# Kernel optimization log

Hardware: AMD Instinct MI355X
Metric: run time of the kernel (lower is better)

## Reference

```python
import jax, jax.numpy as jnp
import numpy as np

Z_DIM = 64
HIDDEN = 400
DATASET = 1000000
EPS = 0.01
S_STEPS = 20
T_STEPS = 5
LOG_2PI = float(np.log(2.0 * np.pi))


def setup_inputs() -> dict:
    key = jax.random.key(0)
    ks = jax.random.split(key, 10)
    B = 16384
    x = jax.random.uniform(ks[0], (B, 1, 28, 28), dtype=jnp.float32)
    indices = jax.random.randint(ks[1], (B,), 0, DATASET, dtype=jnp.int64)
    # MLP params (torch Linear convention: y = x @ W.T + b)
    W1 = jax.random.normal(ks[2], (HIDDEN, 784), dtype=jnp.float32) * 0.03
    b1 = jnp.zeros((HIDDEN,), dtype=jnp.float32)
    W21 = jax.random.normal(ks[3], (Z_DIM, HIDDEN), dtype=jnp.float32) * 0.05
    b21 = jnp.zeros((Z_DIM,), dtype=jnp.float32)
    W22 = jax.random.normal(ks[4], (Z_DIM, HIDDEN), dtype=jnp.float32) * 0.05
    b22 = jnp.zeros((Z_DIM,), dtype=jnp.float32)
    cached_samples = jax.random.normal(ks[5], (DATASET, Z_DIM), dtype=jnp.float32)
    # pre-drawn Langevin noise for all s+t steps
    noise = jax.random.normal(ks[6], (S_STEPS + T_STEPS, B, Z_DIM), dtype=jnp.float32)
    return {"x": x, "indices": indices, "K": 1, "W1": W1, "b1": b1,
            "W21": W21, "b21": b21, "W22": W22, "b22": b22,
            "cached_samples": cached_samples, "noise": noise}


def _encode(x, W1, b1, W21, b21, W22, b22):
    xf = x.reshape(-1, 784)
    h = jax.nn.relu(xf @ W1.T + b1)
    z_loc = h @ W21.T + b21
    z_scale = jnp.exp(h @ W22.T + b22)
    return z_loc, z_scale


def _langevin(z0, noise_steps, z_loc, z_scale):
    # ULA: z <- z + eps * grad_log_q(z) + sqrt(2*eps) * xi
    inv_var = 1.0 / (z_scale * z_scale)
    coef = jnp.sqrt(2.0 * EPS).astype(z0.dtype)

    def step(z, xi):
        grad = (z_loc - z) * inv_var
        return z + EPS * grad + coef * xi, None

    z, _ = jax.lax.scan(step, z0, noise_steps)
    return z


def reference(x, indices, K, W1, b1, W21, b21, W22, b22, cached_samples, noise):
    z_loc, z_scale = _encode(x, W1, b1, W21, b21, W22, b22)
    # gather cached particles
    z = cached_samples[indices]
    # s detached steps, then t graph-carrying steps (same math in fwd)
    z = jax.lax.stop_gradient(_langevin(z, noise[:S_STEPS], z_loc, z_scale))
    z = _langevin(z, noise[S_STEPS:], z_loc, z_scale)
    # scatter updated particles back
    new_cache = cached_samples.at[indices].set(jax.lax.stop_gradient(z))
    # Normal log-prob summed over latent dim
    log_qz_x = jnp.sum(
        -0.5 * jnp.square((z - z_loc) / z_scale) - jnp.log(z_scale) - 0.5 * LOG_2PI,
        axis=-1)
    return log_qz_x, z, new_cache
```

## Files before the change

### kernel.cpp

```cpp
#include <hip/hip_runtime.h>


#define ZD 64
#define NSTEPS 25
#define EPSI 0.01f
#define K1 784
#define K1P 800
#define HSTR 512

typedef __attribute__((ext_vector_type(8))) short short8;
typedef __attribute__((ext_vector_type(4))) float f32x4;

__device__ __forceinline__ unsigned short f2bf(float f) {
  union { float f; unsigned u; } v; v.f = f;
  return (unsigned short)((v.u + 0x7FFFu + ((v.u >> 16) & 1u)) >> 16);
}

__device__ __forceinline__ void gload_lds16(const void* g, void* l) {
  __builtin_amdgcn_global_load_lds(
      (const __attribute__((address_space(1))) void*)g,
      (__attribute__((address_space(3))) void*)l, 16, 0, 0);
}

__global__ __launch_bounds__(256) void prep_kernel(
    const float* __restrict__ W1, const float* __restrict__ W21,
    const float* __restrict__ W22, short* __restrict__ W1b,
    short* __restrict__ Wout) {
  const int t = blockIdx.x * 256 + threadIdx.x;
  const int NW1 = 512 * (K1P / 8);
  if (t < NW1) {
    const int n = t / (K1P / 8), k0 = (t % (K1P / 8)) * 8;
    short8 v = {0, 0, 0, 0, 0, 0, 0, 0};
    if (n < 400 && k0 < K1) {
      const float* s = W1 + (long)n * K1 + k0;
#pragma unroll
      for (int e = 0; e < 8; e++) v[e] = (short)f2bf(s[e]);
    }
    *(short8*)(W1b + (long)t * 8) = v;
  } else {
    const int q = t - NW1;
    if (q < 128 * 64) {
      const int n = q / 64, k0 = (q % 64) * 8;
      short8 v = {0, 0, 0, 0, 0, 0, 0, 0};
      if (k0 < 400) {
        const float* s = (n < 64) ? (W21 + (long)n * 400 + k0)
                                  : (W22 + (long)(n - 64) * 400 + k0);
#pragma unroll
        for (int e = 0; e < 8; e++) v[e] = (short)f2bf(s[e]);
      }
      *(short8*)(Wout + (long)q * 8) = v;
    }
  }
}

__global__ __launch_bounds__(256) void zero_touched_kernel(
    const int* __restrict__ idx, int* __restrict__ winner, int B) {
  const int j = blockIdx.x * 256 + threadIdx.x;
  if (j < B) winner[idx[j]] = 0;
}

__global__ __launch_bounds__(256) void winner_kernel(
    const int* __restrict__ idx, int* __restrict__ winner, int B) {
  const int j = blockIdx.x * 256 + threadIdx.x;
  if (j < B) atomicMax(&winner[idx[j]], j + 1);
}

__global__ __launch_bounds__(256) void gemm1_kernel(
    const float* __restrict__ X, const short* __restrict__ W1b,
    const float* __restrict__ b1, unsigned short* __restrict__ H) {
  __shared__ short As[2 * 64 * 8];
  __shared__ short Bs[16 * 64 * 8];
  const int tid = threadIdx.x;
  const int w = tid >> 6;
  const int lane = tid & 63;
  const int m0 = (blockIdx.x >> 1) * 32;
  const int n0 = (blockIdx.x & 1) * 256;

  const f32x4 vzero = {0.f, 0.f, 0.f, 0.f};
  f32x4 acc[2][4];
#pragma unroll
  for (int i = 0; i < 2; i++)
#pragma unroll
    for (int j = 0; j < 4; j++) acc[i][j] = vzero;

  for (int k0 = 0; k0 < K1P; k0 += 32) {
    if (k0) __syncthreads();
    if (tid < 128) {
      const int row = m0 + (tid >> 6) * 16 + (lane & 15);
      const int gk = k0 + (lane >> 4) * 8;
      short8 av = {0, 0, 0, 0, 0, 0, 0, 0};
      if (gk < K1) {
        const float4 f0 = *(const float4*)(X + (long)row * K1 + gk);
        const float4 f1 = *(const float4*)(X + (long)row * K1 + gk + 4);
        av[0] = (short)f2bf(f0.x); av[1] = (short)f2bf(f0.y);
        av[2] = (short)f2bf(f0.z); av[3] = (short)f2bf(f0.w);
        av[4] = (short)f2bf(f1.x); av[5] = (short)f2bf(f1.y);
        av[6] = (short)f2bf(f1.z); av[7] = (short)f2bf(f1.w);
      }
      *(short8*)(As + (long)tid * 8) = av;
    }
#pragma unroll
    for (int t = 0; t < 4; t++) {
      const int gn = w * 4 + t;
      const short* src = W1b + (long)(n0 + gn * 16 + (lane & 15)) * K1P +
                         k0 + (lane >> 4) * 8;
      gload_lds16(src, Bs + gn * 512);
    }
    __syncthreads();
    const short8* Ap = (const short8*)As;
    const short8* Bp = (const short8*)Bs;
    const short8 a0 = Ap[0 * 64 + lane];
    const short8 a1 = Ap[1 * 64 + lane];
#pragma unroll
    for (int j = 0; j < 4; j++) {
      const short8 b = Bp[(w * 4 + j) * 64 + lane];
      acc[0][j] = __builtin_amdgcn_mfma_f32_16x16x32_bf16(a0, b, acc[0][j], 0, 0, 0);
      acc[1][j] = __builtin_amdgcn_mfma_f32_16x16x32_bf16(a1, b, acc[1][j], 0, 0, 0);
    }
  }
  const int colg = lane & 15;
  const int rowg = (lane >> 4) * 4;
#pragma unroll
  for (int j = 0; j < 4; j++) {
    const int col = n0 + w * 64 + j * 16 + colg;
    const float bias = (col < 400) ? b1[col] : 0.f;
#pragma unroll
    for (int i = 0; i < 2; i++) {
      const int rbase = m0 + i * 16 + rowg;
#pragma unroll
      for (int r = 0; r < 4; r++) {
        H[(long)(rbase + r) * HSTR + col] = f2bf(fmaxf(acc[i][j][r] + bias, 0.f));
      }
    }
  }
}

__global__ __launch_bounds__(256) void gemm2_kernel(
    const unsigned short* __restrict__ H, const short* __restrict__ Wout,
    const float* __restrict__ b21, const float* __restrict__ b22,
    float* __restrict__ zloc, float* __restrict__ uarr) {
  __shared__ short As[2 * 64 * 8];
  __shared__ short Bs[8 * 64 * 8];
  const int tid = threadIdx.x;
  const int w = tid >> 6;
  const int lane = tid & 63;
  const int m0 = blockIdx.x * 32;

  const f32x4 vzero = {0.f, 0.f, 0.f, 0.f};
  f32x4 acc[2][2];
#pragma unroll
  for (int i = 0; i < 2; i++)
#pragma unroll
    for (int j = 0; j < 2; j++) acc[i][j] = vzero;

  for (int k0 = 0; k0 < HSTR; k0 += 32) {
    if (k0) __syncthreads();
    if (w < 2) {
      const unsigned short* src = H + (long)(m0 + w * 16 + (lane & 15)) * HSTR +
                                  k0 + (lane >> 4) * 8;
      gload_lds16(src, As + w * 512);
    }
#pragma unroll
    for (int t = 0; t < 2; t++) {
      const int gn = w * 2 + t;
      const short* src = Wout + (long)(gn * 16 + (lane & 15)) * HSTR +
                         k0 + (lane >> 4) * 8;
      gload_lds16(src, Bs + gn * 512);
    }
    __syncthreads();
    const short8* Ap = (const short8*)As;
    const short8* Bp = (const short8*)Bs;
    const short8 a0 = Ap[0 * 64 + lane];
    const short8 a1 = Ap[1 * 64 + lane];
#pragma unroll
    for (int j = 0; j < 2; j++) {
      const short8 b = Bp[(w * 2 + j) * 64 + lane];
      acc[0][j] = __builtin_amdgcn_mfma_f32_16x16x32_bf16(a0, b, acc[0][j], 0, 0, 0);
      acc[1][j] = __builtin_amdgcn_mfma_f32_16x16x32_bf16(a1, b, acc[1][j], 0, 0, 0);
    }
  }
  const int colg = lane & 15;
  const int rowg = (lane >> 4) * 4;
  float* outp = (w < 2) ? zloc : uarr;
  const float* bp = (w < 2) ? b21 : b22;
#pragma unroll
  for (int j = 0; j < 2; j++) {
    const int col = (w & 1) * 32 + j * 16 + colg;
    const float bias = bp[col];
#pragma unroll
    for (int i = 0; i < 2; i++) {
      const int rbase = m0 + i * 16 + rowg;
#pragma unroll
      for (int r = 0; r < 4; r++) {
        outp[(long)(rbase + r) * ZD + col] = acc[i][j][r] + bias;
      }
    }
  }
}

__global__ __launch_bounds__(256) void copy_kernel(
    const f32x4* __restrict__ src, f32x4* __restrict__ dst) {
  const long e = (long)blockIdx.x * 256 + threadIdx.x;
  dst[e] = src[e];
}

__global__ __launch_bounds__(256) void langevin_kernel(
    const float* __restrict__ zloc, const float* __restrict__ uarr,
    const float* __restrict__ cache, const int* __restrict__ idx,
    const float* __restrict__ noise, const int* __restrict__ winner,
    float* __restrict__ out_logq, float* __restrict__ out_z,
    float* __restrict__ out_cache, int B) {
  const int row = blockIdx.x * 4 + (threadIdx.x >> 6);
  const int lane = threadIdx.x & 63;
  const int i = idx[row];
  const float zl = zloc[(long)row * ZD + lane];
  const float uu = uarr[(long)row * ZD + lane];
  const float a = EPSI * expf(-2.f * uu);
  float z = cache[(long)i * ZD + lane];
  const float coef = sqrtf(2.f * EPSI);
  const float* np = noise + (long)row * ZD + lane;
  const long stride = (long)B * ZD;
#pragma unroll
  for (int s = 0; s < NSTEPS; s++) {
    z = z + a * (zl - z) + coef * np[(long)s * stride];
  }
  out_z[(long)row * ZD + lane] = z;
  if (winner[i] == row + 1) {
    out_cache[(long)i * ZD + lane] = z;
  }
  const float d = (z - zl) * expf(-uu);
  float t = -0.5f * d * d - uu - 0.91893853320467274178f;
#pragma unroll
  for (int off = 1; off < 64; off <<= 1) t += __shfl_xor(t, off);
  if (lane == 0) out_logq[row] = t;
}

extern "C" void kernel_launch(void* const* d_in, const int* in_sizes, int n_in,
                              void* d_out, int out_size, void* d_ws, size_t ws_size,
                              hipStream_t stream) {
  const float* x     = (const float*)d_in[0];
  const int*   idx   = (const int*)d_in[1];
  const float* W1    = (const float*)d_in[3];
  const float* b1    = (const float*)d_in[4];
  const float* W21   = (const float*)d_in[5];
  const float* b21   = (const float*)d_in[6];
  const float* W22   = (const float*)d_in[7];
  const float* b22   = (const float*)d_in[8];
  const float* cache = (const float*)d_in[9];
  const float* noise = (const float*)d_in[10];

  const int B  = in_sizes[1];
  const int DS = in_sizes[9] / ZD;

  float* out_logq  = (float*)d_out;
  float* out_z     = out_logq + B;
  float* out_cache = out_z + (long)B * ZD;

  unsigned short* h = (unsigned short*)d_ws;
  short* w1b  = (short*)(h + (long)B * HSTR);
  short* wout = w1b + 512 * K1P;
  float* zloc = (float*)(wout + 128 * HSTR);
  float* u    = zloc + (long)B * ZD;
  int*   win  = (int*)(u + (long)B * ZD);

  const int prep_chunks = 512 * (K1P / 8) + 128 * 64;
  prep_kernel<<<(prep_chunks + 255) / 256, 256, 0, stream>>>(W1, W21, W22, w1b, wout);
  zero_touched_kernel<<<(B + 255) / 256, 256, 0, stream>>>(idx, win, B);
  winner_kernel<<<(B + 255) / 256, 256, 0, stream>>>(idx, win, B);

  gemm1_kernel<<<(B / 32) * 2, 256, 0, stream>>>(x, w1b, b1, h);
  gemm2_kernel<<<B / 32, 256, 0, stream>>>(h, wout, b21, b22, zloc, u);

  const long n4 = (long)DS * (ZD / 4);
  copy_kernel<<<(unsigned)(n4 / 256), 256, 0, stream>>>(
      (const f32x4*)cache, (f32x4*)out_cache);

  langevin_kernel<<<B / 4, 256, 0, stream>>>(zloc, u, cache, idx, noise, win,
                                             out_logq, out_z, out_cache, B);
}
```

Baseline: 200.1 us.

## Restructure gemm1 to stage full X tile in LDS and stream MFMA-packed weights

gemm1 now uses 512-thread blocks over 64 rows covering all 512 output columns. The whole 64x800 bf16 X tile is converted once into LDS, and the weights are pre-packed by prep_kernel into MFMA fragment order so they can be read straight from global memory (L2-resident) without per-k-step barriers. This removes the duplicate X loads that came from splitting N across two blocks, and it removes the 25 sync/LDS-staging rounds for W1. The cost is 100KB of LDS per block, which limits occupancy. Separately, the cache copy kernel is unrolled to 4 vectors per thread, giving fewer blocks and more loads in flight.

```diff
diff --git a/kernel.cpp b/kernel.cpp
--- a/kernel.cpp
+++ b/kernel.cpp
@@ -5,7 +5,6 @@
 #define NSTEPS 25
 #define EPSI 0.01f
 #define K1 784
-#define K1P 800
 #define HSTR 512
 
 typedef __attribute__((ext_vector_type(8))) short short8;
@@ -24,19 +23,24 @@
 
 __global__ __launch_bounds__(256) void prep_kernel(
     const float* __restrict__ W1, const float* __restrict__ W21,
-    const float* __restrict__ W22, short* __restrict__ W1b,
+    const float* __restrict__ W22, short* __restrict__ W1p,
     short* __restrict__ Wout) {
   const int t = blockIdx.x * 256 + threadIdx.x;
-  const int NW1 = 512 * (K1P / 8);
+  const int NW1 = 32 * 25 * 64;
   if (t < NW1) {
-    const int n = t / (K1P / 8), k0 = (t % (K1P / 8)) * 8;
+    const int g = t / 1600;
+    const int rem = t - g * 1600;
+    const int kc32 = rem >> 6;
+    const int l = rem & 63;
+    const int col = g * 16 + (l & 15);
+    const int k = kc32 * 32 + (l >> 4) * 8;
     short8 v = {0, 0, 0, 0, 0, 0, 0, 0};
-    if (n < 400 && k0 < K1) {
-      const float* s = W1 + (long)n * K1 + k0;
+    if (col < 400 && k + 8 <= K1) {
+      const float* s = W1 + (long)col * K1 + k;
 #pragma unroll
       for (int e = 0; e < 8; e++) v[e] = (short)f2bf(s[e]);
     }
-    *(short8*)(W1b + (long)t * 8) = v;
+    *(short8*)(W1p + (long)t * 8) = v;
   } else {
     const int q = t - NW1;
     if (q < 128 * 64) {
@@ -65,71 +69,69 @@
   if (j < B) atomicMax(&winner[idx[j]], j + 1);
 }
 
-__global__ __launch_bounds__(256) void gemm1_kernel(
-    const float* __restrict__ X, const short* __restrict__ W1b,
+__global__ __launch_bounds__(512, 2) void gemm1_kernel(
+    const float* __restrict__ X, const short* __restrict__ W1p,
     const float* __restrict__ b1, unsigned short* __restrict__ H) {
-  __shared__ short As[2 * 64 * 8];
-  __shared__ short Bs[16 * 64 * 8];
+  __shared__ short As[6400 * 8];
   const int tid = threadIdx.x;
   const int w = tid >> 6;
   const int lane = tid & 63;
-  const int m0 = (blockIdx.x >> 1) * 32;
-  const int n0 = (blockIdx.x & 1) * 256;
+  const int m0 = blockIdx.x * 64;
+
+  for (int slot = tid; slot < 6400; slot += 512) {
+    const int lp = slot & 63;
+    const int chunk = slot >> 6;
+    const int rg = chunk & 3;
+    const int kc32 = chunk >> 2;
+    const int row = rg * 16 + (lp & 15);
+    const int k = kc32 * 32 + (lp >> 4) * 8;
+    short8 av = {0, 0, 0, 0, 0, 0, 0, 0};
+    if (k + 8 <= K1) {
+      const float4 f0 = *(const float4*)(X + (long)(m0 + row) * K1 + k);
+      const float4 f1 = *(const float4*)(X + (long)(m0 + row) * K1 + k + 4);
+      av[0] = (short)f2bf(f0.x); av[1] = (short)f2bf(f0.y);
+      av[2] = (short)f2bf(f0.z); av[3] = (short)f2bf(f0.w);
+      av[4] = (short)f2bf(f1.x); av[5] = (short)f2bf(f1.y);
+      av[6] = (short)f2bf(f1.z); av[7] = (short)f2bf(f1.w);
+    }
+    *(short8*)(As + (long)slot * 8) = av;
+  }
+  __syncthreads();
 
   const f32x4 vzero = {0.f, 0.f, 0.f, 0.f};
-  f32x4 acc[2][4];
-#pragma unroll
-  for (int i = 0; i < 2; i++)
+  f32x4 acc[4][4];
+#pragma unroll
+  for (int i = 0; i < 4; i++)
 #pragma unroll
     for (int j = 0; j < 4; j++) acc[i][j] = vzero;
 
-  for (int k0 = 0; k0 < K1P; k0 += 32) {
-    if (k0) __syncthreads();
-    if (tid < 128) {
-      const int row = m0 + (tid >> 6) * 16 + (lane & 15);
-      const int gk = k0 + (lane >> 4) * 8;
-      short8 av = {0, 0, 0, 0, 0, 0, 0, 0};
-      if (gk < K1) {
-        const float4 f0 = *(const float4*)(X + (long)row * K1 + gk);
-        const float4 f1 = *(const float4*)(X + (long)row * K1 + gk + 4);
-        av[0] = (short)f2bf(f0.x); av[1] = (short)f2bf(f0.y);
-        av[2] = (short)f2bf(f0.z); av[3] = (short)f2bf(f0.w);
-        av[4] = (short)f2bf(f1.x); av[5] = (short)f2bf(f1.y);
-        av[6] = (short)f2bf(f1.z); av[7] = (short)f2bf(f1.w);
-      }
-      *(short8*)(As + (long)tid * 8) = av;
-    }
-#pragma unroll
-    for (int t = 0; t < 4; t++) {
-      const int gn = w * 4 + t;
-      const short* src = W1b + (long)(n0 + gn * 16 + (lane & 15)) * K1P +
-                         k0 + (lane >> 4) * 8;
-      gload_lds16(src, Bs + gn * 512);
-    }
-    __syncthreads();
-    const short8* Ap = (const short8*)As;
-    const short8* Bp = (const short8*)Bs;
-    const short8 a0 = Ap[0 * 64 + lane];
-    const short8 a1 = Ap[1 * 64 + lane];
-#pragma unroll
-    for (int j = 0; j < 4; j++) {
-      const short8 b = Bp[(w * 4 + j) * 64 + lane];
-      acc[0][j] = __builtin_amdgcn_mfma_f32_16x16x32_bf16(a0, b, acc[0][j], 0, 0, 0);
-      acc[1][j] = __builtin_amdgcn_mfma_f32_16x16x32_bf16(a1, b, acc[1][j], 0, 0, 0);
-    }
-  }
+  const short8* Ap = (const short8*)As;
+  const short8* Bp = (const short8*)W1p;
+  for (int kc = 0; kc < 25; kc++) {
+    short8 a[4], b[4];
+#pragma unroll
+    for (int rg = 0; rg < 4; rg++) a[rg] = Ap[(kc * 4 + rg) * 64 + lane];
+#pragma unroll
+    for (int j = 0; j < 4; j++) b[j] = Bp[((w * 4 + j) * 25 + kc) * 64 + lane];
+#pragma unroll
+    for (int rg = 0; rg < 4; rg++)
+#pragma unroll
+      for (int j = 0; j < 4; j++)
+        acc[rg][j] = __builtin_amdgcn_mfma_f32_16x16x32_bf16(a[rg], b[j], acc[rg][j], 0, 0, 0);
+  }
+
   const int colg = lane & 15;
   const int rowg = (lane >> 4) * 4;
 #pragma unroll
   for (int j = 0; j < 4; j++) {
-    const int col = n0 + w * 64 + j * 16 + colg;
+    const int col = w * 64 + j * 16 + colg;
     const float bias = (col < 400) ? b1[col] : 0.f;
 #pragma unroll
-    for (int i = 0; i < 2; i++) {
-      const int rbase = m0 + i * 16 + rowg;
+    for (int rg = 0; rg < 4; rg++) {
+      const int rbase = m0 + rg * 16 + rowg;
 #pragma unroll
       for (int r = 0; r < 4; r++) {
-        H[(long)(rbase + r) * HSTR + col] = f2bf(fmaxf(acc[i][j][r] + bias, 0.f));
+        H[(long)(rbase + r) * HSTR + col] = f2bf(fmaxf(acc[rg][j][r] + bias, 0.f));
       }
     }
   }
@@ -200,8 +202,15 @@
 
 __global__ __launch_bounds__(256) void copy_kernel(
     const f32x4* __restrict__ src, f32x4* __restrict__ dst) {
-  const long e = (long)blockIdx.x * 256 + threadIdx.x;
-  dst[e] = src[e];
+  const long base = (long)blockIdx.x * 1024 + threadIdx.x;
+  f32x4 v0 = src[base];
+  f32x4 v1 = src[base + 256];
+  f32x4 v2 = src[base + 512];
+  f32x4 v3 = src[base + 768];
+  dst[base] = v0;
+  dst[base + 256] = v1;
+  dst[base + 512] = v2;
+  dst[base + 768] = v3;
 }
 
 __global__ __launch_bounds__(256) void langevin_kernel(
@@ -257,22 +266,22 @@
   float* out_cache = out_z + (long)B * ZD;
 
   unsigned short* h = (unsigned short*)d_ws;
-  short* w1b  = (short*)(h + (long)B * HSTR);
-  short* wout = w1b + 512 * K1P;
+  short* w1p  = (short*)(h + (long)B * HSTR);
+  short* wout = w1p + 32 * 25 * 64 * 8;
   float* zloc = (float*)(wout + 128 * HSTR);
   float* u    = zloc + (long)B * ZD;
   int*   win  = (int*)(u + (long)B * ZD);
 
-  const int prep_chunks = 512 * (K1P / 8) + 128 * 64;
-  prep_kernel<<<(prep_chunks + 255) / 256, 256, 0, stream>>>(W1, W21, W22, w1b, wout);
+  const int prep_chunks = 32 * 25 * 64 + 128 * 64;
+  prep_kernel<<<(prep_chunks + 255) / 256, 256, 0, stream>>>(W1, W21, W22, w1p, wout);
   zero_touched_kernel<<<(B + 255) / 256, 256, 0, stream>>>(idx, win, B);
   winner_kernel<<<(B + 255) / 256, 256, 0, stream>>>(idx, win, B);
 
-  gemm1_kernel<<<(B / 32) * 2, 256, 0, stream>>>(x, w1b, b1, h);
+  gemm1_kernel<<<B / 64, 512, 0, stream>>>(x, w1p, b1, h);
   gemm2_kernel<<<B / 32, 256, 0, stream>>>(h, wout, b21, b22, zloc, u);
 
   const long n4 = (long)DS * (ZD / 4);
-  copy_kernel<<<(unsigned)(n4 / 256), 256, 0, stream>>>(
+  copy_kernel<<<(unsigned)(n4 / 1024), 256, 0, stream>>>(
       (const f32x4*)cache, (f32x4*)out_cache);
 
   langevin_kernel<<<B / 4, 256, 0, stream>>>(zloc, u, cache, idx, noise, win,
```

Measured after the change: 180.7 us. -9.7%, faster.
